# Kernel tuning notes

Measured on AMD Instinct MI355X. Metric: run time of the kernel, lower is better.

Reference implementation:

```python
import jax, jax.numpy as jnp
import numpy as np
from jax import lax

D_MODEL = 768; DEPTH = 12; HEADS = 12; HEAD_D = 64; PATCH = 16; IMG = 224
NTOK = (IMG // PATCH) ** 2 + 1  # 197
BATCH = 32; K_PATCHES = 5; EPS = 1e-6


def setup_inputs() -> dict:
    key = jax.random.key(0)
    ks = jax.random.split(key, 16)
    rn = lambda i, shape, s=1.0: jax.random.normal(ks[i], shape, jnp.float32) * s
    return {
        'x': rn(0, (BATCH, 3, IMG, IMG)),
        'patch_w': rn(1, (D_MODEL, 3, PATCH, PATCH), 0.02),
        'patch_b': jnp.zeros((D_MODEL,), jnp.float32),
        'cls_token': rn(2, (1, 1, D_MODEL), 0.02),
        'pos_embed': rn(3, (1, NTOK, D_MODEL), 0.02),
        'ln1_w': jnp.ones((DEPTH, D_MODEL), jnp.float32),
        'ln1_b': jnp.zeros((DEPTH, D_MODEL), jnp.float32),
        'qkv_w': rn(4, (DEPTH, 3 * D_MODEL, D_MODEL), 0.02),
        'qkv_b': jnp.zeros((DEPTH, 3 * D_MODEL), jnp.float32),
        'proj_w': rn(5, (DEPTH, D_MODEL, D_MODEL), 0.02),
        'proj_b': jnp.zeros((DEPTH, D_MODEL), jnp.float32),
        'pk_param': rn(6, (DEPTH, HEADS, HEAD_D), 0.02),
        'pv_param': rn(7, (DEPTH, HEADS, HEAD_D), 0.02),
        'prompt_k': rn(8, (DEPTH, HEADS, HEAD_D), 0.02),
        'prompt_v': rn(9, (DEPTH, HEADS, HEAD_D), 0.02),
        'ln2_w': jnp.ones((DEPTH, D_MODEL), jnp.float32),
        'ln2_b': jnp.zeros((DEPTH, D_MODEL), jnp.float32),
        'fc1_w': rn(10, (DEPTH, 4 * D_MODEL, D_MODEL), 0.02),
        'fc1_b': jnp.zeros((DEPTH, 4 * D_MODEL), jnp.float32),
        'fc2_w': rn(11, (DEPTH, D_MODEL, 4 * D_MODEL), 0.02),
        'fc2_b': jnp.zeros((DEPTH, D_MODEL), jnp.float32),
        'norm_w': jnp.ones((D_MODEL,), jnp.float32),
        'norm_b': jnp.zeros((D_MODEL,), jnp.float32),
        'k_patches': K_PATCHES,
    }


def _layer_norm(h, w, b):
    mu = h.mean(-1, keepdims=True)
    var = ((h - mu) ** 2).mean(-1, keepdims=True)
    return (h - mu) * lax.rsqrt(var + EPS) * w + b


def reference(x, patch_w, patch_b, cls_token, pos_embed, ln1_w, ln1_b, qkv_w, qkv_b,
              proj_w, proj_b, pk_param, pv_param, prompt_k, prompt_v, ln2_w, ln2_b,
              fc1_w, fc1_b, fc2_w, fc2_b, norm_w, norm_b, k_patches):
    B = x.shape[0]
    C, H, D = D_MODEL, HEADS, HEAD_D
    scale = D ** -0.5
    # patch embedding: conv stride=patch -> [B, C, 14, 14] -> [B, 196, C]
    p = lax.conv_general_dilated(x, patch_w, (PATCH, PATCH), 'VALID',
                                 dimension_numbers=('NCHW', 'OIHW', 'NCHW'))
    p = p.reshape(B, C, -1).transpose(0, 2, 1) + patch_b
    tokens = jnp.concatenate([jnp.broadcast_to(cls_token, (B, 1, C)), p], axis=1) + pos_embed
    N = tokens.shape[1]
    batch_idx = jnp.arange(B)[:, None]

    for l in range(DEPTH):
        h = _layer_norm(tokens, ln1_w[l], ln1_b[l])
        qkv = (h @ qkv_w[l].T + qkv_b[l]).reshape(B, N, 3, H, D).transpose(2, 0, 3, 1, 4)
        q, k, v = qkv[0], qkv[1], qkv[2]  # [B,H,N,D]
        # probe attention: softmax is row-wise, only the CLS row is used downstream
        probe = jax.nn.softmax(jnp.einsum('bhd,bhkd->bhk', q[:, :, 0], k) * scale, axis=-1)
        cls_scores = probe.mean(axis=1)[:, 1:]  # [B, N-1]
        topk_idx = lax.top_k(cls_scores, k_patches)[1] + 1  # [B, k] in [1, N)
        sel = jnp.zeros((B, N), tokens.dtype).at[batch_idx, topk_idx].add(1.0)  # [B,N]
        # prompt override of CLS k/v + scatter-add of learned patch prompts at top-k patches
        k_mod = k.at[:, :, 0, :].add(prompt_k[l]) + sel[:, None, :, None] * pk_param[l][None, :, None, :]
        v_mod = v.at[:, :, 0, :].add(prompt_v[l]) + sel[:, None, :, None] * pv_param[l][None, :, None, :]
        attn = jax.nn.softmax(jnp.einsum('bhqd,bhkd->bhqk', q, k_mod) * scale, axis=-1)
        out = jnp.einsum('bhqk,bhkd->bhqd', attn, v_mod).transpose(0, 2, 1, 3).reshape(B, N, C)
        tokens = tokens + (out @ proj_w[l].T + proj_b[l])
        h2 = _layer_norm(tokens, ln2_w[l], ln2_b[l])
        m = jax.nn.gelu(h2 @ fc1_w[l].T + fc1_b[l], approximate=False) @ fc2_w[l].T + fc2_b[l]
        tokens = tokens + m

    return _layer_norm(tokens, norm_w, norm_b)
```

## Files before the change

kernel.cpp:

```cpp
#include <hip/hip_runtime.h>
#include <math.h>

#define DMODEL 768
#define DEPTH 12
#define HEADS 12
#define HEADD 64
#define NTOK 197
#define BATCH 32
#define NPATCH 196
#define MTOK (BATCH * NTOK)
#define MPAT (BATCH * NPATCH)
#define QKVD 2304
#define MLPD 3072

typedef unsigned short u16;
typedef __attribute__((ext_vector_type(8))) short bf16x8;
typedef __attribute__((ext_vector_type(4))) float f32x4;

#define OFF_QKV 0
#define OFF_PROJ (QKVD * DMODEL)
#define OFF_FC1 (OFF_PROJ + DMODEL * DMODEL)
#define OFF_FC2 (OFF_FC1 + MLPD * DMODEL)
#define WTOTAL (OFF_FC2 + DMODEL * MLPD)

__device__ __forceinline__ u16 bf16r(float x) {
  union { float f; unsigned u; } c; c.f = x;
  unsigned u = c.u + 0x7FFF + ((c.u >> 16) & 1);
  return (u16)(u >> 16);
}
__device__ __forceinline__ float gelu_f(float x) {
  return 0.5f * x * (1.f + erff(x * 0.70710678118654752440f));
}
__device__ __forceinline__ void gload16(const void* g, void* l) {
  __builtin_amdgcn_global_load_lds(
      (const __attribute__((address_space(1))) void*)g,
      (__attribute__((address_space(3))) void*)l, 16, 0, 0);
}

__device__ __forceinline__ float blk_red_sum(float v, float* red) {
#pragma unroll
  for (int o = 32; o; o >>= 1) v += __shfl_xor(v, o);
  __syncthreads();
  if ((threadIdx.x & 63) == 0) red[threadIdx.x >> 6] = v;
  __syncthreads();
  return red[0] + red[1] + red[2] + red[3];
}
__device__ __forceinline__ float blk_red_max(float v, float* red) {
#pragma unroll
  for (int o = 32; o; o >>= 1) v = fmaxf(v, __shfl_xor(v, o));
  __syncthreads();
  if ((threadIdx.x & 63) == 0) red[threadIdx.x >> 6] = v;
  __syncthreads();
  return fmaxf(fmaxf(red[0], red[1]), fmaxf(red[2], red[3]));
}

__global__ __launch_bounds__(256) void convert_bf16(const float* __restrict__ in,
                                                    u16* __restrict__ out, int n) {
  int i = (blockIdx.x * 256 + threadIdx.x) * 4;
  if (i >= n) return;
  float4 v = *(const float4*)(in + i);
  ushort4 o;
  o.x = bf16r(v.x); o.y = bf16r(v.y); o.z = bf16r(v.z); o.w = bf16r(v.w);
  *(ushort4*)(out + i) = o;
}

__global__ __launch_bounds__(256) void convert_layer_w(
    const float* __restrict__ qkv_w, const float* __restrict__ proj_w,
    const float* __restrict__ fc1_w, const float* __restrict__ fc2_w,
    u16* __restrict__ wbuf) {
  int i = (blockIdx.x * 256 + threadIdx.x) * 4;
  if (i >= WTOTAL) return;
  const float* s;
  if (i < OFF_PROJ) s = qkv_w + i;
  else if (i < OFF_FC1) s = proj_w + (i - OFF_PROJ);
  else if (i < OFF_FC2) s = fc1_w + (i - OFF_FC1);
  else s = fc2_w + (i - OFF_FC2);
  float4 v = *(const float4*)s;
  ushort4 o;
  o.x = bf16r(v.x); o.y = bf16r(v.y); o.z = bf16r(v.z); o.w = bf16r(v.w);
  *(ushort4*)(wbuf + i) = o;
}

__global__ __launch_bounds__(256) void convert_all_w(
    const float* __restrict__ qkv_w, const float* __restrict__ proj_w,
    const float* __restrict__ fc1_w, const float* __restrict__ fc2_w,
    u16* __restrict__ wall) {
  const int l = blockIdx.y;
  int i = (blockIdx.x * 256 + threadIdx.x) * 4;
  if (i >= WTOTAL) return;
  const float* s;
  if (i < OFF_PROJ) s = qkv_w + (size_t)l * QKVD * DMODEL + i;
  else if (i < OFF_FC1) s = proj_w + (size_t)l * DMODEL * DMODEL + (i - OFF_PROJ);
  else if (i < OFF_FC2) s = fc1_w + (size_t)l * MLPD * DMODEL + (i - OFF_FC1);
  else s = fc2_w + (size_t)l * DMODEL * MLPD + (i - OFF_FC2);
  float4 v = *(const float4*)s;
  ushort4 o;
  o.x = bf16r(v.x); o.y = bf16r(v.y); o.z = bf16r(v.z); o.w = bf16r(v.w);
  *(ushort4*)(wall + (size_t)l * WTOTAL + i) = o;
}

__global__ __launch_bounds__(256) void im2col(const float* __restrict__ x,
                                              u16* __restrict__ col) {
  int idx = blockIdx.x * 256 + threadIdx.x;
  if (idx >= MPAT * DMODEL) return;
  int kk = idx % DMODEL;
  int m = idx / DMODEL;
  int bb = m / NPATCH, p = m % NPATCH;
  int ph = p / 14, pw = p % 14;
  int ch = kk >> 8, rem = kk & 255;
  int i = rem >> 4, j = rem & 15;
  col[idx] = bf16r(x[(((size_t)bb * 3 + ch) * 224 + ph * 16 + i) * 224 + pw * 16 + j]);
}

__global__ __launch_bounds__(256) void assemble(const float* __restrict__ pat,
                                                const float* __restrict__ cls,
                                                const float* __restrict__ pos,
                                                float* __restrict__ tokens) {
  int idx = blockIdx.x * 256 + threadIdx.x;
  if (idx >= MTOK * DMODEL) return;
  int c = idx % DMODEL;
  int t = idx / DMODEL;
  int bb = t / NTOK, n = t % NTOK;
  float v;
  if (n == 0) v = cls[c];
  else v = pat[((size_t)bb * NPATCH + (n - 1)) * DMODEL + c];
  tokens[idx] = v + pos[n * DMODEL + c];
}

template <bool BF16OUT>
__global__ __launch_bounds__(256) void layernorm_w(const float* __restrict__ in,
                                                   const float* __restrict__ w,
                                                   const float* __restrict__ b,
                                                   void* __restrict__ outp,
                                                   int ntok) {
  const int wv = threadIdx.x >> 6, lane = threadIdx.x & 63;
  const int t = blockIdx.x * 4 + wv;
  if (t >= ntok) return;
  const f32x4* r = (const f32x4*)(in + (size_t)t * DMODEL);
  f32x4 x0 = r[lane], x1 = r[lane + 64], x2 = r[lane + 128];
  float s = (x0[0] + x0[1] + x0[2] + x0[3]) + (x1[0] + x1[1] + x1[2] + x1[3]) +
            (x2[0] + x2[1] + x2[2] + x2[3]);
#pragma unroll
  for (int o = 32; o; o >>= 1) s += __shfl_xor(s, o);
  const float mu = s * (1.f / 768.f);
  float vs = 0.f;
#pragma unroll
  for (int e = 0; e < 4; ++e) {
    float d0 = x0[e] - mu, d1 = x1[e] - mu, d2 = x2[e] - mu;
    vs += d0 * d0 + d1 * d1 + d2 * d2;
  }
#pragma unroll
  for (int o = 32; o; o >>= 1) vs += __shfl_xor(vs, o);
  const float is = rsqrtf(vs * (1.f / 768.f) + 1e-6f);
  const f32x4* wp = (const f32x4*)w;
  const f32x4* bp = (const f32x4*)b;
  f32x4 w0 = wp[lane], w1 = wp[lane + 64], w2 = wp[lane + 128];
  f32x4 b0 = bp[lane], b1 = bp[lane + 64], b2 = bp[lane + 128];
  f32x4 y0, y1, y2;
#pragma unroll
  for (int e = 0; e < 4; ++e) {
    y0[e] = (x0[e] - mu) * is * w0[e] + b0[e];
    y1[e] = (x1[e] - mu) * is * w1[e] + b1[e];
    y2[e] = (x2[e] - mu) * is * w2[e] + b2[e];
  }
  if (BF16OUT) {
    ushort4* o = (ushort4*)((u16*)outp + (size_t)t * DMODEL);
    ushort4 q0, q1, q2;
#pragma unroll
    for (int e = 0; e < 4; ++e) {
      ((u16*)&q0)[e] = bf16r(y0[e]);
      ((u16*)&q1)[e] = bf16r(y1[e]);
      ((u16*)&q2)[e] = bf16r(y2[e]);
    }
    o[lane] = q0; o[lane + 64] = q1; o[lane + 128] = q2;
  } else {
    f32x4* o = (f32x4*)((float*)outp + (size_t)t * DMODEL);
    o[lane] = y0; o[lane + 64] = y1; o[lane + 128] = y2;
  }
}

template <int MODE, int TN>
__global__ __launch_bounds__(256) void gemm3(const u16* __restrict__ A,
                                             const u16* __restrict__ B,
                                             const float* __restrict__ bias,
                                             void* __restrict__ C,
                                             int M, int N, int K) {
  constexpr int NJ = TN / 32;
  constexpr int LPT = (TN == 128) ? 4 : 3;
  __shared__ u16 As[3][128 * 32];
  __shared__ u16 Bs[3][TN * 32];
  const int tid = threadIdx.x;
  const int w = tid >> 6, lane = tid & 63;

  const int nwg = gridDim.x * gridDim.y;
  int lin = blockIdx.y * gridDim.x + blockIdx.x;
  {
    int q = nwg >> 3, r = nwg & 7;
    int xcd = lin & 7, idx = lin >> 3;
    lin = (xcd < r ? xcd * (q + 1) : r * (q + 1) + (xcd - r) * q) + idx;
  }
  const int ntn = gridDim.y;
  const int m0 = (lin / ntn) * 128, n0 = (lin % ntn) * TN;

  const int wr = (w >> 1) * 64, wc = (w & 1) * (TN / 2);
  f32x4 acc[4][NJ] = {};

  const int srow = tid >> 2;
  const int scol = ((tid & 3) ^ ((srow >> 1) & 3)) * 8;
  int ar0 = m0 + srow;       if (ar0 >= M) ar0 = M - 1;
  int ar1 = m0 + 64 + srow;  if (ar1 >= M) ar1 = M - 1;
  const u16* Ag0 = A + (size_t)ar0 * K + scol;
  const u16* Ag1 = A + (size_t)ar1 * K + scol;
  const u16* Bg0 = B + (size_t)(n0 + srow) * K + scol;
  const u16* Bg1 = B + (size_t)(n0 + (TN == 128 ? 64 : 0) + srow) * K + scol;

  auto STAGE = [&](int buf, int kk) {
    gload16(Ag0 + kk, &As[buf][w * 512]);
    gload16(Ag1 + kk, &As[buf][2048 + w * 512]);
    gload16(Bg0 + kk, &Bs[buf][w * 512]);
    if (TN == 128) gload16(Bg1 + kk, &Bs[buf][2048 + w * 512]);
  };

  const int fr = lane & 15, lq = lane >> 4;
  const int kq = (lq ^ ((fr >> 1) & 3)) * 8;

  const int nt = K >> 5;
  STAGE(0, 0);
  STAGE(1, 32);
  asm volatile("s_waitcnt vmcnt(%0)" ::"n"(LPT) : "memory");
  __builtin_amdgcn_s_barrier();
  __builtin_amdgcn_sched_barrier(0);

  for (int t = 0; t < nt; ++t) {
    const int cur = t % 3;
    bf16x8 af[4], bfr[NJ];
#pragma unroll
    for (int i = 0; i < 4; ++i)
      af[i] = *(const bf16x8*)&As[cur][(wr + i * 16 + fr) * 32 + kq];
#pragma unroll
    for (int j = 0; j < NJ; ++j)
      bfr[j] = *(const bf16x8*)&Bs[cur][(wc + j * 16 + fr) * 32 + kq];
    const bool more = (t + 2 < nt);
    if (more) STAGE((t + 2) % 3, (t + 2) * 32);
#pragma unroll
    for (int i = 0; i < 4; ++i)
#pragma unroll
      for (int j = 0; j < NJ; ++j)
        acc[i][j] = __builtin_amdgcn_mfma_f32_16x16x32_bf16(af[i], bfr[j],
                                                            acc[i][j], 0, 0, 0);
    if (more)
      asm volatile("s_waitcnt vmcnt(%0)" ::"n"(LPT) : "memory");
    else
      asm volatile("s_waitcnt vmcnt(0)" ::: "memory");
    __builtin_amdgcn_s_barrier();
    __builtin_amdgcn_sched_barrier(0);
  }

  const int fq = lq * 4;
#pragma unroll
  for (int j = 0; j < NJ; ++j) {
    const int n = n0 + wc + j * 16 + fr;
    const float bb = bias[n];
#pragma unroll
    for (int i = 0; i < 4; ++i) {
      const int mbase = m0 + wr + i * 16 + fq;
#pragma unroll
      for (int r = 0; r < 4; ++r) {
        const int m = mbase + r;
        if (m < M) {
          const float v = acc[i][j][r] + bb;
          if (MODE == 0) ((float*)C)[(size_t)m * N + n] = v;
          else if (MODE == 1) ((float*)C)[(size_t)m * N + n] += v;
          else ((u16*)C)[(size_t)m * N + n] = bf16r(gelu_f(v));
        }
      }
    }
  }
}

__global__ __launch_bounds__(256) void probe_scores(const float* __restrict__ qkv,
                                                    float* __restrict__ probs) {
  __shared__ float qrow[64];
  __shared__ float s[NTOK];
  __shared__ float red[4];
  const int bh = blockIdx.x;
  const int b = bh / HEADS, h = bh % HEADS;
  const int tid = threadIdx.x;
  const size_t row0 = (size_t)b * NTOK * QKVD;
  if (tid < 64) qrow[tid] = qkv[row0 + h * HEADD + tid];
  __syncthreads();
  const int sub = tid & 3;
  for (int k = tid >> 2; k < NTOK; k += 64) {
    const float* kr = qkv + row0 + (size_t)k * QKVD + DMODEL + h * HEADD + sub * 16;
    float dot = 0.f;
#pragma unroll
    for (int c = 0; c < 4; ++c) {
      float4 kv = *(const float4*)(kr + c * 4);
      dot = fmaf(qrow[sub * 16 + c * 4 + 0], kv.x, dot);
      dot = fmaf(qrow[sub * 16 + c * 4 + 1], kv.y, dot);
      dot = fmaf(qrow[sub * 16 + c * 4 + 2], kv.z, dot);
      dot = fmaf(qrow[sub * 16 + c * 4 + 3], kv.w, dot);
    }
    dot += __shfl_xor(dot, 1);
    dot += __shfl_xor(dot, 2);
    if (sub == 0) s[k] = dot * 0.125f;
  }
  __syncthreads();
  float mx = -1e30f;
  for (int k = tid; k < NTOK; k += 256) mx = fmaxf(mx, s[k]);
  mx = blk_red_max(mx, red);
  float sm = 0.f;
  for (int k = tid; k < NTOK; k += 256) sm += expf(s[k] - mx);
  sm = blk_red_sum(sm, red);
  float inv = 1.f / sm;
  for (int k = tid; k < NTOK; k += 256)
    probs[(size_t)bh * NTOK + k] = expf(s[k] - mx) * inv;
}

__global__ __launch_bounds__(256) void topk_sel(const float* __restrict__ probs,
                                                const int* __restrict__ kpptr,
                                                int* __restrict__ topk) {
  __shared__ float accsc[NTOK];
  const int b = blockIdx.x, tid = threadIdx.x;
  for (int k = tid; k < NTOK; k += 256) {
    float a = 0.f;
#pragma unroll
    for (int h = 0; h < HEADS; ++h) a += probs[(size_t)(b * HEADS + h) * NTOK + k];
    accsc[k] = a;
  }
  __syncthreads();
  if (tid == 0) {
    int kpn = kpptr[0];
    if (kpn < 0) kpn = 0;
    if (kpn > 8) kpn = 8;
    for (int j = 0; j < kpn; ++j) {
      float best = -1e30f;
      int bi = 1;
      for (int k = 1; k < NTOK; ++k)
        if (accsc[k] > best) { best = accsc[k]; bi = k; }
      topk[b * 8 + j] = bi;
      accsc[bi] = -2e30f;
    }
    for (int j = kpn; j < 8; ++j) topk[b * 8 + j] = -1;
  }
}

__device__ __forceinline__ bf16x8 pack8(float4 a, float4 b) {
  bf16x8 r;
  r[0] = (short)bf16r(a.x); r[1] = (short)bf16r(a.y);
  r[2] = (short)bf16r(a.z); r[3] = (short)bf16r(a.w);
  r[4] = (short)bf16r(b.x); r[5] = (short)bf16r(b.y);
  r[6] = (short)bf16r(b.z); r[7] = (short)bf16r(b.w);
  return r;
}

__global__ __launch_bounds__(512, 1) void attn_mfma(
    const float* __restrict__ qkv, const float* __restrict__ prompt_k,
    const float* __restrict__ prompt_v, const float* __restrict__ pk,
    const float* __restrict__ pv, const int* __restrict__ topk,
    const int* __restrict__ kpptr, u16* __restrict__ outp) {
  __shared__ u16 Ks[208 * 64];
  __shared__ u16 Vs[64 * 256];
  __shared__ u16 Ps[8][16 * 256];
  __shared__ float selb[NTOK];
  const int bh = blockIdx.x;
  const int b = bh / HEADS, h = bh % HEADS;
  const int tid = threadIdx.x, w = tid >> 6, lane = tid & 63;
  const int fr = lane & 15, lq = lane >> 4;

  int kpn = kpptr[0];
  if (kpn < 0) kpn = 0;
  if (kpn > 8) kpn = 8;
  for (int k = tid; k < NTOK; k += 512) {
    float sl = 0.f;
    for (int j = 0; j < kpn; ++j)
      if (topk[b * 8 + j] == k) sl = 1.f;
    selb[k] = sl;
  }
  __syncthreads();

  const size_t row0 = (size_t)b * NTOK * QKVD;
  const float* kg = qkv + row0 + DMODEL + h * HEADD;
  const float* vg = qkv + row0 + 2 * DMODEL + h * HEADD;
  for (int idx = tid; idx < 208 * 64; idx += 512) {
    int tok = idx >> 6, d = idx & 63;
    float v = 0.f;
    if (tok < NTOK) {
      v = kg[(size_t)tok * QKVD + d] + selb[tok] * pk[h * HEADD + d];
      if (tok == 0) v += prompt_k[h * HEADD + d];
    }
    int off = (tok * 128 + d * 2) ^ ((tok & 7) << 4);
    *(u16*)((char*)Ks + off) = bf16r(v);
  }
  for (int idx = tid; idx < 224 * 64; idx += 512) {
    int tok = idx >> 6, d = idx & 63;
    float v = 0.f;
    if (tok < NTOK) {
      v = vg[(size_t)tok * QKVD + d] + selb[tok] * pv[h * HEADD + d];
      if (tok == 0) v += prompt_v[h * HEADD + d];
    }
    int off = (d * 512 + tok * 2) ^ ((d & 7) << 4);
    *(u16*)((char*)Vs + off) = bf16r(v);
  }
  __syncthreads();

  u16* Pw = Ps[w];
  u16* ob = outp + (size_t)b * NTOK * DMODEL + h * HEADD;

#pragma unroll
  for (int pass = 0; pass < 2; ++pass) {
    const int qt = pass * 8 + w;
    const bool active = (qt < 14);
    if (active) {
      int qrow = qt * 16 + fr;
      if (qrow > NTOK - 1) qrow = NTOK - 1;
      const float* qp = qkv + row0 + (size_t)qrow * QKVD + h * HEADD + lq * 8;
      bf16x8 aq0 = pack8(*(const float4*)qp, *(const float4*)(qp + 4));
      bf16x8 aq1 = pack8(*(const float4*)(qp + 32), *(const float4*)(qp + 36));
      f32x4 sa[13];
#pragma unroll
      for (int j = 0; j < 13; ++j) {
        int tok = j * 16 + fr;
        int o0 = (tok * 128 + lq * 16) ^ ((tok & 7) << 4);
        int o1 = (tok * 128 + 64 + lq * 16) ^ ((tok & 7) << 4);
        bf16x8 bk0 = *(const bf16x8*)((const char*)Ks + o0);
        bf16x8 bk1 = *(const bf16x8*)((const char*)Ks + o1);
        f32x4 z = {0.f, 0.f, 0.f, 0.f};
        z = __builtin_amdgcn_mfma_f32_16x16x32_bf16(aq0, bk0, z, 0, 0, 0);
        sa[j] = __builtin_amdgcn_mfma_f32_16x16x32_bf16(aq1, bk1, z, 0, 0, 0);
      }
      const bool v12 = (fr < 5);
      float m4[4] = {-1e30f, -1e30f, -1e30f, -1e30f};
#pragma unroll
      for (int j = 0; j < 13; ++j) {
        if (j == 12 && !v12) continue;
#pragma unroll
        for (int r = 0; r < 4; ++r) m4[r] = fmaxf(m4[r], sa[j][r] * 0.125f);
      }
#pragma unroll
      for (int o = 8; o; o >>= 1)
#pragma unroll
        for (int r = 0; r < 4; ++r) m4[r] = fmaxf(m4[r], __shfl_xor(m4[r], o));
      float s4[4] = {0.f, 0.f, 0.f, 0.f};
#pragma unroll
      for (int j = 0; j < 13; ++j) {
        const bool valid = (j < 12) || v12;
#pragma unroll
        for (int r = 0; r < 4; ++r) {
          float p = valid ? __expf(sa[j][r] * 0.125f - m4[r]) : 0.f;
          sa[j][r] = p;
          s4[r] += p;
        }
      }
#pragma unroll
      for (int o = 8; o; o >>= 1)
#pragma unroll
        for (int r = 0; r < 4; ++r) s4[r] += __shfl_xor(s4[r], o);
      float inv[4];
#pragma unroll
      for (int r = 0; r < 4; ++r) inv[r] = 1.f / s4[r];
#pragma unroll
      for (int r = 0; r < 4; ++r) {
        int row = lq * 4 + r;
        int rbase = row * 512, sw = (row & 7) << 4;
#pragma unroll
        for (int j = 0; j < 13; ++j) {
          int off = (rbase + (j * 16 + fr) * 2) ^ sw;
          *(u16*)((char*)Pw + off) = bf16r(sa[j][r] * inv[r]);
        }
        int offz = (rbase + (208 + fr) * 2) ^ sw;
        *(u16*)((char*)Pw + offz) = 0;
      }
    }
    __syncthreads();
    if (active) {
      f32x4 oa[4] = {};
#pragma unroll
      for (int kc = 0; kc < 7; ++kc) {
        int po = (fr * 512 + (kc * 32 + lq * 8) * 2) ^ ((fr & 7) << 4);
        bf16x8 pa = *(const bf16x8*)((const char*)Pw + po);
#pragma unroll
        for (int dt = 0; dt < 4; ++dt) {
          int d = dt * 16 + fr;
          int vo = (d * 512 + (kc * 32 + lq * 8) * 2) ^ ((d & 7) << 4);
          bf16x8 vb = *(const bf16x8*)((const char*)Vs + vo);
          oa[dt] = __builtin_amdgcn_mfma_f32_16x16x32_bf16(pa, vb, oa[dt], 0, 0, 0);
        }
      }
#pragma unroll
      for (int r = 0; r < 4; ++r) {
        int q = qt * 16 + lq * 4 + r;
        if (q < NTOK) {
          u16* orow = ob + (size_t)q * DMODEL;
#pragma unroll
          for (int dt = 0; dt < 4; ++dt) orow[dt * 16 + fr] = bf16r(oa[dt][r]);
        }
      }
    }
    __syncthreads();
  }
}

extern "C" void kernel_launch(void* const* d_in, const int* in_sizes, int n_in,
                              void* d_out, int out_size, void* d_ws, size_t ws_size,
                              hipStream_t stream) {
  const float* x = (const float*)d_in[0];
  const float* patch_w = (const float*)d_in[1];
  const float* patch_b = (const float*)d_in[2];
  const float* cls_tok = (const float*)d_in[3];
  const float* pos_emb = (const float*)d_in[4];
  const float* ln1_w = (const float*)d_in[5];
  const float* ln1_b = (const float*)d_in[6];
  const float* qkv_w = (const float*)d_in[7];
  const float* qkv_b = (const float*)d_in[8];
  const float* proj_w = (const float*)d_in[9];
  const float* proj_b = (const float*)d_in[10];
  const float* pk_par = (const float*)d_in[11];
  const float* pv_par = (const float*)d_in[12];
  const float* pr_k = (const float*)d_in[13];
  const float* pr_v = (const float*)d_in[14];
  const float* ln2_w = (const float*)d_in[15];
  const float* ln2_b = (const float*)d_in[16];
  const float* fc1_w = (const float*)d_in[17];
  const float* fc1_b = (const float*)d_in[18];
  const float* fc2_w = (const float*)d_in[19];
  const float* fc2_b = (const float*)d_in[20];
  const float* norm_w = (const float*)d_in[21];
  const float* norm_b = (const float*)d_in[22];
  const int* kp = (const int*)d_in[23];

  char* base = (char*)d_ws;
  float* tokens = (float*)base;
  float* bufh = (float*)(base + 19365888ull);
  float* bufbig = (float*)(base + 38731776ull);
  u16* im2colb = (u16*)(base + 116195328ull);
  u16* patchwb = (u16*)(base + 125829120ull);
  int* topk = (int*)(base + 127008768ull);
  float* probs = (float*)(base + 127009792ull);
  u16* wbuf = (u16*)(base + 127312384ull);
  const size_t WBYTES = (size_t)WTOTAL * 2;
  const bool batch = ws_size >= 127312384ull + WBYTES * DEPTH;

  const int mt = (MTOK + 127) / 128;
  const int mtp = (MPAT + 127) / 128;
  const int lnb = (MTOK + 3) / 4;

  if (batch)
    convert_all_w<<<dim3(WTOTAL / 1024, DEPTH), 256, 0, stream>>>(
        qkv_w, proj_w, fc1_w, fc2_w, wbuf);

  convert_bf16<<<(DMODEL * DMODEL / 4 + 255) / 256, 256, 0, stream>>>(
      patch_w, patchwb, DMODEL * DMODEL);
  im2col<<<(MPAT * DMODEL + 255) / 256, 256, 0, stream>>>(x, im2colb);
  gemm3<0, 64><<<dim3(mtp, DMODEL / 64), 256, 0, stream>>>(
      im2colb, patchwb, patch_b, bufh, MPAT, DMODEL, DMODEL);
  assemble<<<(MTOK * DMODEL + 255) / 256, 256, 0, stream>>>(bufh, cls_tok,
                                                            pos_emb, tokens);

  for (int l = 0; l < DEPTH; ++l) {
    u16* wl = batch ? (wbuf + (size_t)l * WTOTAL) : wbuf;
    if (!batch)
      convert_layer_w<<<(WTOTAL / 4 + 255) / 256, 256, 0, stream>>>(
          qkv_w + (size_t)l * QKVD * DMODEL,
          proj_w + (size_t)l * DMODEL * DMODEL,
          fc1_w + (size_t)l * MLPD * DMODEL,
          fc2_w + (size_t)l * DMODEL * MLPD, wl);
    layernorm_w<true><<<lnb, 256, 0, stream>>>(tokens, ln1_w + l * DMODEL,
                                               ln1_b + l * DMODEL, bufh, MTOK);
    gemm3<0, 128><<<dim3(mt, QKVD / 128), 256, 0, stream>>>(
        (const u16*)bufh, wl + OFF_QKV, qkv_b + l * QKVD, bufbig,
        MTOK, QKVD, DMODEL);
    probe_scores<<<BATCH * HEADS, 256, 0, stream>>>(bufbig, probs);
    topk_sel<<<BATCH, 256, 0, stream>>>(probs, kp, topk);
    attn_mfma<<<BATCH * HEADS, 512, 0, stream>>>(
        bufbig, pr_k + l * HEADS * HEADD, pr_v + l * HEADS * HEADD,
        pk_par + l * HEADS * HEADD, pv_par + l * HEADS * HEADD, topk, kp,
        (u16*)bufh);
    gemm3<1, 64><<<dim3(mt, DMODEL / 64), 256, 0, stream>>>(
        (const u16*)bufh, wl + OFF_PROJ, proj_b + l * DMODEL, tokens,
        MTOK, DMODEL, DMODEL);
    layernorm_w<true><<<lnb, 256, 0, stream>>>(tokens, ln2_w + l * DMODEL,
                                               ln2_b + l * DMODEL, bufh, MTOK);
    gemm3<2, 128><<<dim3(mt, MLPD / 128), 256, 0, stream>>>(
        (const u16*)bufh, wl + OFF_FC1, fc1_b + l * MLPD, bufbig,
        MTOK, MLPD, DMODEL);
    gemm3<1, 64><<<dim3(mt, DMODEL / 64), 256, 0, stream>>>(
        (const u16*)bufbig, wl + OFF_FC2, fc2_b + l * DMODEL, tokens,
        MTOK, DMODEL, MLPD);
  }
  layernorm_w<false><<<lnb, 256, 0, stream>>>(tokens, norm_w, norm_b, d_out,
                                              MTOK);
}
```

Before: 3.783 ms.

## Store QKV output in bf16 and deepen GEMM pipeline to four stages

The QKV projection now writes its output as bf16 instead of fp32, and the probe and attention kernels read that bf16 buffer directly. This halves the traffic for the largest intermediate and drops the per-load fp32-to-bf16 packing in attention. Separately, the GEMM grows from three to four LDS buffers and keeps three K-tiles in flight, with vmcnt waits adjusted to match. The cost is more LDS per block, which may lower occupancy, plus slightly less precise probe scores, which could flip near-tied top-k choices.

Result: slower. 3.897 ms (+3.0%).

```diff
diff --git a/kernel.cpp b/kernel.cpp
--- a/kernel.cpp
+++ b/kernel.cpp
@@ -27,6 +27,11 @@
   union { float f; unsigned u; } c; c.f = x;
   unsigned u = c.u + 0x7FFF + ((c.u >> 16) & 1);
   return (u16)(u >> 16);
+}
+__device__ __forceinline__ float bf2f(u16 h) {
+  union { unsigned u; float f; } c;
+  c.u = (unsigned)h << 16;
+  return c.f;
 }
 __device__ __forceinline__ float gelu_f(float x) {
   return 0.5f * x * (1.f + erff(x * 0.70710678118654752440f));
@@ -180,15 +185,15 @@
 }
 
 template <int MODE, int TN>
-__global__ __launch_bounds__(256) void gemm3(const u16* __restrict__ A,
+__global__ __launch_bounds__(256) void gemm4(const u16* __restrict__ A,
                                              const u16* __restrict__ B,
                                              const float* __restrict__ bias,
                                              void* __restrict__ C,
                                              int M, int N, int K) {
   constexpr int NJ = TN / 32;
   constexpr int LPT = (TN == 128) ? 4 : 3;
-  __shared__ u16 As[3][128 * 32];
-  __shared__ u16 Bs[3][TN * 32];
+  __shared__ u16 As[4][128 * 32];
+  __shared__ u16 Bs[4][TN * 32];
   const int tid = threadIdx.x;
   const int w = tid >> 6, lane = tid & 63;
 
@@ -227,12 +232,13 @@
   const int nt = K >> 5;
   STAGE(0, 0);
   STAGE(1, 32);
-  asm volatile("s_waitcnt vmcnt(%0)" ::"n"(LPT) : "memory");
+  STAGE(2, 64);
+  asm volatile("s_waitcnt vmcnt(%0)" ::"n"(2 * LPT) : "memory");
   __builtin_amdgcn_s_barrier();
   __builtin_amdgcn_sched_barrier(0);
 
   for (int t = 0; t < nt; ++t) {
-    const int cur = t % 3;
+    const int cur = t & 3;
     bf16x8 af[4], bfr[NJ];
 #pragma unroll
     for (int i = 0; i < 4; ++i)
@@ -240,15 +246,18 @@
 #pragma unroll
     for (int j = 0; j < NJ; ++j)
       bfr[j] = *(const bf16x8*)&Bs[cur][(wc + j * 16 + fr) * 32 + kq];
-    const bool more = (t + 2 < nt);
-    if (more) STAGE((t + 2) % 3, (t + 2) * 32);
+    if (t + 3 < nt) STAGE((t + 3) & 3, (t + 3) * 32);
 #pragma unroll
     for (int i = 0; i < 4; ++i)
 #pragma unroll
       for (int j = 0; j < NJ; ++j)
         acc[i][j] = __builtin_amdgcn_mfma_f32_16x16x32_bf16(af[i], bfr[j],
                                                             acc[i][j], 0, 0, 0);
-    if (more)
+    const int lim = (t + 3 < nt - 1) ? t + 3 : nt - 1;
+    const int inflight = lim - t - 1;
+    if (inflight >= 2)
+      asm volatile("s_waitcnt vmcnt(%0)" ::"n"(2 * LPT) : "memory");
+    else if (inflight == 1)
       asm volatile("s_waitcnt vmcnt(%0)" ::"n"(LPT) : "memory");
     else
       asm volatile("s_waitcnt vmcnt(0)" ::: "memory");
@@ -271,14 +280,15 @@
           const float v = acc[i][j][r] + bb;
           if (MODE == 0) ((float*)C)[(size_t)m * N + n] = v;
           else if (MODE == 1) ((float*)C)[(size_t)m * N + n] += v;
-          else ((u16*)C)[(size_t)m * N + n] = bf16r(gelu_f(v));
+          else if (MODE == 2) ((u16*)C)[(size_t)m * N + n] = bf16r(gelu_f(v));
+          else ((u16*)C)[(size_t)m * N + n] = bf16r(v);
         }
       }
     }
   }
 }
 
-__global__ __launch_bounds__(256) void probe_scores(const float* __restrict__ qkv,
+__global__ __launch_bounds__(256) void probe_scores(const u16* __restrict__ qkv,
                                                     float* __restrict__ probs) {
   __shared__ float qrow[64];
   __shared__ float s[NTOK];
@@ -287,19 +297,18 @@
   const int b = bh / HEADS, h = bh % HEADS;
   const int tid = threadIdx.x;
   const size_t row0 = (size_t)b * NTOK * QKVD;
-  if (tid < 64) qrow[tid] = qkv[row0 + h * HEADD + tid];
+  if (tid < 64) qrow[tid] = bf2f(qkv[row0 + h * HEADD + tid]);
   __syncthreads();
   const int sub = tid & 3;
   for (int k = tid >> 2; k < NTOK; k += 64) {
-    const float* kr = qkv + row0 + (size_t)k * QKVD + DMODEL + h * HEADD + sub * 16;
+    const u16* kr = qkv + row0 + (size_t)k * QKVD + DMODEL + h * HEADD + sub * 16;
+    bf16x8 k0 = *(const bf16x8*)kr;
+    bf16x8 k1 = *(const bf16x8*)(kr + 8);
     float dot = 0.f;
 #pragma unroll
-    for (int c = 0; c < 4; ++c) {
-      float4 kv = *(const float4*)(kr + c * 4);
-      dot = fmaf(qrow[sub * 16 + c * 4 + 0], kv.x, dot);
-      dot = fmaf(qrow[sub * 16 + c * 4 + 1], kv.y, dot);
-      dot = fmaf(qrow[sub * 16 + c * 4 + 2], kv.z, dot);
-      dot = fmaf(qrow[sub * 16 + c * 4 + 3], kv.w, dot);
+    for (int e = 0; e < 8; ++e) {
+      dot = fmaf(qrow[sub * 16 + e], bf2f((u16)k0[e]), dot);
+      dot = fmaf(qrow[sub * 16 + 8 + e], bf2f((u16)k1[e]), dot);
     }
     dot += __shfl_xor(dot, 1);
     dot += __shfl_xor(dot, 2);
@@ -345,17 +354,8 @@
   }
 }
 
-__device__ __forceinline__ bf16x8 pack8(float4 a, float4 b) {
-  bf16x8 r;
-  r[0] = (short)bf16r(a.x); r[1] = (short)bf16r(a.y);
-  r[2] = (short)bf16r(a.z); r[3] = (short)bf16r(a.w);
-  r[4] = (short)bf16r(b.x); r[5] = (short)bf16r(b.y);
-  r[6] = (short)bf16r(b.z); r[7] = (short)bf16r(b.w);
-  return r;
-}
-
 __global__ __launch_bounds__(512, 1) void attn_mfma(
-    const float* __restrict__ qkv, const float* __restrict__ prompt_k,
+    const u16* __restrict__ qkv, const float* __restrict__ prompt_k,
     const float* __restrict__ prompt_v, const float* __restrict__ pk,
     const float* __restrict__ pv, const int* __restrict__ topk,
     const int* __restrict__ kpptr, u16* __restrict__ outp) {
@@ -380,13 +380,13 @@
   __syncthreads();
 
   const size_t row0 = (size_t)b * NTOK * QKVD;
-  const float* kg = qkv + row0 + DMODEL + h * HEADD;
-  const float* vg = qkv + row0 + 2 * DMODEL + h * HEADD;
+  const u16* kg = qkv + row0 + DMODEL + h * HEADD;
+  const u16* vg = qkv + row0 + 2 * DMODEL + h * HEADD;
   for (int idx = tid; idx < 208 * 64; idx += 512) {
     int tok = idx >> 6, d = idx & 63;
     float v = 0.f;
     if (tok < NTOK) {
-      v = kg[(size_t)tok * QKVD + d] + selb[tok] * pk[h * HEADD + d];
+      v = bf2f(kg[(size_t)tok * QKVD + d]) + selb[tok] * pk[h * HEADD + d];
       if (tok == 0) v += prompt_k[h * HEADD + d];
     }
     int off = (tok * 128 + d * 2) ^ ((tok & 7) << 4);
@@ -396,7 +396,7 @@
     int tok = idx >> 6, d = idx & 63;
     float v = 0.f;
     if (tok < NTOK) {
-      v = vg[(size_t)tok * QKVD + d] + selb[tok] * pv[h * HEADD + d];
+      v = bf2f(vg[(size_t)tok * QKVD + d]) + selb[tok] * pv[h * HEADD + d];
       if (tok == 0) v += prompt_v[h * HEADD + d];
     }
     int off = (d * 512 + tok * 2) ^ ((d & 7) << 4);
@@ -414,9 +414,9 @@
     if (active) {
       int qrow = qt * 16 + fr;
       if (qrow > NTOK - 1) qrow = NTOK - 1;
-      const float* qp = qkv + row0 + (size_t)qrow * QKVD + h * HEADD + lq * 8;
-      bf16x8 aq0 = pack8(*(const float4*)qp, *(const float4*)(qp + 4));
-      bf16x8 aq1 = pack8(*(const float4*)(qp + 32), *(const float4*)(qp + 36));
+      const u16* qp = qkv + row0 + (size_t)qrow * QKVD + h * HEADD + lq * 8;
+      bf16x8 aq0 = *(const bf16x8*)qp;
+      bf16x8 aq1 = *(const bf16x8*)(qp + 32);
       f32x4 sa[13];
 #pragma unroll
       for (int j = 0; j < 13; ++j) {
@@ -552,7 +552,7 @@
   convert_bf16<<<(DMODEL * DMODEL / 4 + 255) / 256, 256, 0, stream>>>(
       patch_w, patchwb, DMODEL * DMODEL);
   im2col<<<(MPAT * DMODEL + 255) / 256, 256, 0, stream>>>(x, im2colb);
-  gemm3<0, 64><<<dim3(mtp, DMODEL / 64), 256, 0, stream>>>(
+  gemm4<0, 64><<<dim3(mtp, DMODEL / 64), 256, 0, stream>>>(
       im2colb, patchwb, patch_b, bufh, MPAT, DMODEL, DMODEL);
   assemble<<<(MTOK * DMODEL + 255) / 256, 256, 0, stream>>>(bufh, cls_tok,
                                                             pos_emb, tokens);
@@ -567,24 +567,24 @@
           fc2_w + (size_t)l * DMODEL * MLPD, wl);
     layernorm_w<true><<<lnb, 256, 0, stream>>>(tokens, ln1_w + l * DMODEL,
                                                ln1_b + l * DMODEL, bufh, MTOK);
-    gemm3<0, 128><<<dim3(mt, QKVD / 128), 256, 0, stream>>>(
+    gemm4<3, 128><<<dim3(mt, QKVD / 128), 256, 0, stream>>>(
         (const u16*)bufh, wl + OFF_QKV, qkv_b + l * QKVD, bufbig,
         MTOK, QKVD, DMODEL);
-    probe_scores<<<BATCH * HEADS, 256, 0, stream>>>(bufbig, probs);
+    probe_scores<<<BATCH * HEADS, 256, 0, stream>>>((const u16*)bufbig, probs);
     topk_sel<<<BATCH, 256, 0, stream>>>(probs, kp, topk);
     attn_mfma<<<BATCH * HEADS, 512, 0, stream>>>(
-        bufbig, pr_k + l * HEADS * HEADD, pr_v + l * HEADS * HEADD,
+        (const u16*)bufbig, pr_k + l * HEADS * HEADD, pr_v + l * HEADS * HEADD,
         pk_par + l * HEADS * HEADD, pv_par + l * HEADS * HEADD, topk, kp,
         (u16*)bufh);
-    gemm3<1, 64><<<dim3(mt, DMODEL / 64), 256, 0, stream>>>(
+    gemm4<1, 64><<<dim3(mt, DMODEL / 64), 256, 0, stream>>>(
         (const u16*)bufh, wl + OFF_PROJ, proj_b + l * DMODEL, tokens,
         MTOK, DMODEL, DMODEL);
     layernorm_w<true><<<lnb, 256, 0, stream>>>(tokens, ln2_w + l * DMODEL,
                                                ln2_b + l * DMODEL, bufh, MTOK);
-    gemm3<2, 128><<<dim3(mt, MLPD / 128), 256, 0, stream>>>(
+    gemm4<2, 128><<<dim3(mt, MLPD / 128), 256, 0, stream>>>(
         (const u16*)bufh, wl + OFF_FC1, fc1_b + l * MLPD, bufbig,
         MTOK, MLPD, DMODEL);
-    gemm3<1, 64><<<dim3(mt, DMODEL / 64), 256, 0, stream>>>(
+    gemm4<1, 64><<<dim3(mt, DMODEL / 64), 256, 0, stream>>>(
         (const u16*)bufbig, wl + OFF_FC2, fc2_b + l * DMODEL, tokens,
         MTOK, DMODEL, MLPD);
   }
```
